# Kernel tuning notes

Measured on AMD Instinct MI355X. Metric: run time of the kernel, lower is better.

Reference implementation:

```python
import jax, jax.numpy as jnp
import numpy as np

HIDDEN = 4096
NUM_EXPERTS = 64
TOP_K = 2


def setup_inputs() -> dict:
    key = jax.random.key(0)
    k1, k2, k3 = jax.random.split(key, 3)
    hidden_states = jax.random.normal(k1, (4, 4096, HIDDEN), dtype=jnp.float32)
    # nn.Linear(hidden_size, num_experts): weight [num_experts, hidden], bias [num_experts]
    bound = 1.0 / np.sqrt(HIDDEN)
    gate_w = jax.random.uniform(k2, (NUM_EXPERTS, HIDDEN), dtype=jnp.float32, minval=-bound, maxval=bound)
    gate_b = jax.random.uniform(k3, (NUM_EXPERTS,), dtype=jnp.float32, minval=-bound, maxval=bound)
    return {"hidden_states": hidden_states, "gate_w": gate_w, "gate_b": gate_b}


def reference(hidden_states, gate_w, gate_b):
    b, s, h = hidden_states.shape
    x = hidden_states.reshape(-1, h)                      # [N, H], N = b*s
    router_logits = jnp.einsum('nh,eh->ne', x, gate_w) + gate_b  # [N, E]
    top_logits, selected_experts = jax.lax.top_k(router_logits, TOP_K)  # [N, K]
    routing_weights = jax.nn.softmax(top_logits, axis=-1)  # [N, K]
    aux_loss = jnp.float32(0.0)
    return routing_weights, selected_experts, router_logits, aux_loss
```

## Files before the change

kernel.cpp:

```cpp
#include <hip/hip_runtime.h>
#include <math.h>
#include <stdint.h>

#define HIDDEN 4096
#define NEXP   64
#define TOKS   64
#define KBLK   2048
#define KCH    64
#define NCHK   (KBLK / KCH)
#define X_FL   (TOKS * KCH)
#define PAR_FL (X_FL + 2 * 2048)

typedef __bf16 bf16x8 __attribute__((ext_vector_type(8)));
typedef float  f32x4  __attribute__((ext_vector_type(4)));

union BfU { uint4 u; bf16x8 b; };

static __device__ __forceinline__ void cvt_hilo(const float* x8, bf16x8& hi, bf16x8& lo) {
#pragma unroll
    for (int j = 0; j < 8; ++j) {
        const float x = x8[j];
        const __bf16 h = (__bf16)x;
        const float  r = x - (float)h;
        hi[j] = h;
        lo[j] = (__bf16)r;
    }
}

__device__ __forceinline__ void gload_lds16(const void* g, void* l) {
    __builtin_amdgcn_global_load_lds(
        (const __attribute__((address_space(1))) void*)g,
        (__attribute__((address_space(3))) void*)l, 16, 0, 0);
}

__global__ __launch_bounds__(512) void wconv_kernel(
    const float* __restrict__ W, ushort* __restrict__ wsHi, ushort* __restrict__ wsLo)
{
    const int gid = blockIdx.x * blockDim.x + threadIdx.x;
    const int S = gid >> 8;
    const int e = (gid >> 6) & 3;
    const int l = gid & 63;
    const int row = 16 * e + (l & 15);
    const int k0  = 32 * S + 8 * (l >> 4);
    const float* src = W + (size_t)row * HIDDEN + k0;
    float x8[8];
    *(float4*)&x8[0] = *(const float4*)src;
    *(float4*)&x8[4] = *(const float4*)(src + 4);
    BfU hi, lo;
    cvt_hilo(x8, hi.b, lo.b);
    const size_t o = ((size_t)(S * 4 + e) * 64 + l) * 8;
    *(uint4*)(wsHi + o) = hi.u;
    *(uint4*)(wsLo + o) = lo.u;
}

__global__ __launch_bounds__(512, 2) void gemm_half_kernel(
    const float* __restrict__ X,
    const ushort* __restrict__ wsHi, const ushort* __restrict__ wsLo,
    float* __restrict__ outLog, float* __restrict__ wsP, int nTok)
{
    __shared__ float smem[2 * PAR_FL];

    const int tid = threadIdx.x;
    const int wv  = tid >> 6;
    const int tg  = wv >> 1;
    const int kh  = wv & 1;
    const int l   = tid & 63;
    const int g   = l >> 4;
    const int cr  = l & 15;
    const int bx  = blockIdx.x;
    const int h   = bx & 1;
    const int t0  = (bx >> 1) * TOKS;

    const float* XgS[2];
    int xdst[2];
#pragma unroll
    for (int r = 0; r < 2; ++r) {
        const int q    = 2 * wv + r;
        const int srow = 4 * q + (l >> 4);
        const int sgr  = (l & 8) | ((l & 7) ^ (srow & 7));
        XgS[r]  = X + (size_t)(t0 + srow) * HIDDEN + h * KBLK + sgr * 4;
        xdst[r] = 4 * q * KCH;
    }
    const ushort* BhS = wsHi + (size_t)h * 131072 + (size_t)wv * 512 + (size_t)l * 8;
    const ushort* BlS = wsLo + (size_t)h * 131072 + (size_t)wv * 512 + (size_t)l * 8;
    const int bhdst = X_FL + wv * 256;
    const int bldst = X_FL + 2048 + wv * 256;

    const int m8   = cr & 7;
    const int rowX = (16 * tg + cr) * KCH;
    const int gA0  = (8 * kh + ((2 * g + 0) ^ m8)) << 2;
    const int gA1  = (8 * kh + ((2 * g + 1) ^ m8)) << 2;

    f32x4 acc[4] = {{0.f,0.f,0.f,0.f},{0.f,0.f,0.f,0.f},{0.f,0.f,0.f,0.f},{0.f,0.f,0.f,0.f}};

#pragma unroll
    for (int r = 0; r < 2; ++r) gload_lds16(XgS[r], smem + xdst[r]);
    gload_lds16(BhS, smem + bhdst);
    gload_lds16(BlS, smem + bldst);
#pragma unroll
    for (int r = 0; r < 2; ++r) gload_lds16(XgS[r] + KCH, smem + PAR_FL + xdst[r]);
    gload_lds16(BhS + 4096, smem + PAR_FL + bhdst);
    gload_lds16(BlS + 4096, smem + PAR_FL + bldst);

#pragma unroll 1
    for (int c = 0; c < NCHK; ++c) {
        if (c + 1 < NCHK) asm volatile("s_waitcnt vmcnt(4)" ::: "memory");
        else              asm volatile("s_waitcnt vmcnt(0)" ::: "memory");
        __builtin_amdgcn_s_barrier();
        const int p = c & 1;
        {
            const float*  xb = smem + p * PAR_FL;
            const ushort* bh = (const ushort*)(xb + X_FL) + (4 * kh) * 512 + l * 8;
            const ushort* bl = bh + 4096;
            float x8[8];
            *(float4*)&x8[0] = *(const float4*)(xb + rowX + gA0);
            *(float4*)&x8[4] = *(const float4*)(xb + rowX + gA1);
            bf16x8 xh, xo; cvt_hilo(x8, xh, xo);
#pragma unroll
            for (int e = 0; e < 4; ++e) {
                BfU ph, pl;
                ph.u = *(const uint4*)(bh + e * 512);
                pl.u = *(const uint4*)(bl + e * 512);
                acc[e] = __builtin_amdgcn_mfma_f32_16x16x32_bf16(xh, ph.b, acc[e], 0, 0, 0);
                acc[e] = __builtin_amdgcn_mfma_f32_16x16x32_bf16(xo, ph.b, acc[e], 0, 0, 0);
                acc[e] = __builtin_amdgcn_mfma_f32_16x16x32_bf16(xh, pl.b, acc[e], 0, 0, 0);
            }
        }
        __builtin_amdgcn_s_barrier();
        if (c + 2 < NCHK) {
            float* pb = smem + p * PAR_FL;
            const int ko = (c + 2) * KCH;
            const size_t bo = (size_t)(c + 2) * 4096;
#pragma unroll
            for (int r = 0; r < 2; ++r) gload_lds16(XgS[r] + ko, pb + xdst[r]);
            gload_lds16(BhS + bo, pb + bhdst);
            gload_lds16(BlS + bo, pb + bldst);
        }
    }

    __syncthreads();

    float (*tiles)[64][68] = (float (*)[64][68])smem;
#pragma unroll
    for (int e = 0; e < 4; ++e)
#pragma unroll
        for (int i = 0; i < 4; ++i)
            tiles[kh][16 * tg + 4 * g + i][16 * e + cr] = acc[e][i];
    __syncthreads();

    {
        float* dst = (h ? wsP : outLog) + (size_t)t0 * NEXP;
        const int tok = tid >> 3;
        const int e8  = (tid & 7) * 8;
        float v[8];
#pragma unroll
        for (int j = 0; j < 8; ++j)
            v[j] = tiles[0][tok][e8 + j] + tiles[1][tok][e8 + j];
        float* rowp = dst + (size_t)tok * NEXP + e8;
        *(float4*)rowp       = make_float4(v[0], v[1], v[2], v[3]);
        *(float4*)(rowp + 4) = make_float4(v[4], v[5], v[6], v[7]);
    }
}

__global__ __launch_bounds__(256) void combine_kernel(
    const float* __restrict__ wsP,
    const float* __restrict__ Bv,
    float* __restrict__ out, int nTok)
{
    __shared__ float tt[64 * 65];
    const int tid = threadIdx.x;
    const int t0  = blockIdx.x * TOKS;
    const size_t offSel = (size_t)nTok * 2;
    const size_t offLog = (size_t)nTok * 4;
    float*       L = out + offLog + (size_t)t0 * NEXP;
    const float* P = wsP + (size_t)t0 * NEXP;

#pragma unroll
    for (int r = 0; r < 4; ++r) {
        const int idx = r * 256 + tid;
        const int tok = idx >> 4;
        const int e4  = (idx & 15) * 4;
        const float4 a  = *(const float4*)(L + tok * NEXP + e4);
        const float4 b  = *(const float4*)(P + tok * NEXP + e4);
        const float4 bb = *(const float4*)(Bv + e4);
        const float4 s = make_float4(a.x + b.x + bb.x, a.y + b.y + bb.y,
                                     a.z + b.z + bb.z, a.w + b.w + bb.w);
        *(float4*)(L + tok * NEXP + e4) = s;
        tt[(e4 + 0) * 65 + tok] = s.x;
        tt[(e4 + 1) * 65 + tok] = s.y;
        tt[(e4 + 2) * 65 + tok] = s.z;
        tt[(e4 + 3) * 65 + tok] = s.w;
    }
    __syncthreads();

    if (tid < 64) {
        const int t = tid;
        float m1 = -INFINITY, m2 = -INFINITY;
        int i1 = 0, i2 = 0;
#pragma unroll
        for (int e = 0; e < NEXP; ++e) {
            const float v = tt[e * 65 + t];
            if (v > m1)      { m2 = m1; i2 = i1; m1 = v; i1 = e; }
            else if (v > m2) { m2 = v; i2 = e; }
        }
        const float ex  = expf(m2 - m1);
        const float inv = 1.0f / (1.0f + ex);
        *(float2*)(out + (size_t)(t0 + tid) * 2)          = make_float2(inv, ex * inv);
        *(float2*)(out + offSel + (size_t)(t0 + tid) * 2) = make_float2((float)i1, (float)i2);
    }

    if (blockIdx.x == 0 && tid == 0)
        out[offLog + (size_t)nTok * NEXP] = 0.0f;
}

extern "C" void kernel_launch(void* const* d_in, const int* in_sizes, int n_in,
                              void* d_out, int out_size, void* d_ws, size_t ws_size,
                              hipStream_t stream)
{
    const float* X  = (const float*)d_in[0];
    const float* W  = (const float*)d_in[1];
    const float* Bv = (const float*)d_in[2];
    float* out = (float*)d_out;
    const int nTok  = in_sizes[0] / HIDDEN;
    const int tiles = nTok / TOKS;
    ushort* wsHi = (ushort*)d_ws;
    ushort* wsLo = wsHi + (size_t)NEXP * HIDDEN;
    float*  wsP  = (float*)(wsLo + (size_t)NEXP * HIDDEN);
    float*  outLog = out + (size_t)nTok * 4;

    wconv_kernel<<<256, 128, 0, stream>>>(W, wsHi, wsLo);
    gemm_half_kernel<<<2 * tiles, 512, 0, stream>>>(X, wsHi, wsLo, outLog, wsP, nTok);
    combine_kernel<<<tiles, 256, 0, stream>>>(wsP, Bv, out, nTok);
}
```

Measured before the change: 67.03 us.

## Split K four ways and divide experts across waves in the gating GEMM

The K dimension is now split into four partial blocks instead of two, giving four times the number of token tiles in blocks. Within a block the waves no longer split K between them; each pair of waves splits the 64 experts, which removes the in-block reduction. Chunks shrink to 32 so shared memory fits more blocks per CU (launch bounds now ask for 4). The cost is three partial logit buffers that the combine kernel must read and sum, which adds extra global traffic.

```diff
diff --git a/kernel.cpp b/kernel.cpp
--- a/kernel.cpp
+++ b/kernel.cpp
@@ -5,11 +5,12 @@
 #define HIDDEN 4096
 #define NEXP   64
 #define TOKS   64
-#define KBLK   2048
-#define KCH    64
+#define NSPLIT 4
+#define KBLK   (HIDDEN / NSPLIT)
+#define KCH    32
 #define NCHK   (KBLK / KCH)
 #define X_FL   (TOKS * KCH)
-#define PAR_FL (X_FL + 2 * 2048)
+#define PAR_FL (X_FL + 2 * 1024)
 
 typedef __bf16 bf16x8 __attribute__((ext_vector_type(8)));
 typedef float  f32x4  __attribute__((ext_vector_type(4)));
@@ -33,7 +34,7 @@
         (__attribute__((address_space(3))) void*)l, 16, 0, 0);
 }
 
-__global__ __launch_bounds__(512) void wconv_kernel(
+__global__ __launch_bounds__(128) void wconv_kernel(
     const float* __restrict__ W, ushort* __restrict__ wsHi, ushort* __restrict__ wsLo)
 {
     const int gid = blockIdx.x * blockDim.x + threadIdx.x;
@@ -53,7 +54,7 @@
     *(uint4*)(wsLo + o) = lo.u;
 }
 
-__global__ __launch_bounds__(512, 2) void gemm_half_kernel(
+__global__ __launch_bounds__(512, 4) void gemm_q_kernel(
     const float* __restrict__ X,
     const ushort* __restrict__ wsHi, const ushort* __restrict__ wsLo,
     float* __restrict__ outLog, float* __restrict__ wsP, int nTok)
@@ -63,61 +64,51 @@
     const int tid = threadIdx.x;
     const int wv  = tid >> 6;
     const int tg  = wv >> 1;
-    const int kh  = wv & 1;
+    const int eh  = wv & 1;
     const int l   = tid & 63;
     const int g   = l >> 4;
     const int cr  = l & 15;
     const int bx  = blockIdx.x;
-    const int h   = bx & 1;
-    const int t0  = (bx >> 1) * TOKS;
-
-    const float* XgS[2];
-    int xdst[2];
-#pragma unroll
-    for (int r = 0; r < 2; ++r) {
-        const int q    = 2 * wv + r;
-        const int srow = 4 * q + (l >> 4);
-        const int sgr  = (l & 8) | ((l & 7) ^ (srow & 7));
-        XgS[r]  = X + (size_t)(t0 + srow) * HIDDEN + h * KBLK + sgr * 4;
-        xdst[r] = 4 * q * KCH;
-    }
-    const ushort* BhS = wsHi + (size_t)h * 131072 + (size_t)wv * 512 + (size_t)l * 8;
-    const ushort* BlS = wsLo + (size_t)h * 131072 + (size_t)wv * 512 + (size_t)l * 8;
-    const int bhdst = X_FL + wv * 256;
-    const int bldst = X_FL + 2048 + wv * 256;
+    const int h   = bx & 3;
+    const int t0  = (bx >> 2) * TOKS;
+
+    const int srow = 8 * wv + (l >> 3);
+    const int sgr  = (l & 7) ^ (l >> 3);
+    const float* XgS = X + (size_t)(t0 + srow) * HIDDEN + h * KBLK + sgr * 4;
+    const int xdst  = wv * 256;
+
+    const ushort* BS = (wv < 4 ? wsHi : wsLo)
+                     + (size_t)h * 65536 + (size_t)(wv & 3) * 512 + (size_t)l * 8;
+    const int bdst = X_FL + (wv < 4 ? 0 : 1024) + (wv & 3) * 256;
 
     const int m8   = cr & 7;
     const int rowX = (16 * tg + cr) * KCH;
-    const int gA0  = (8 * kh + ((2 * g + 0) ^ m8)) << 2;
-    const int gA1  = (8 * kh + ((2 * g + 1) ^ m8)) << 2;
-
-    f32x4 acc[4] = {{0.f,0.f,0.f,0.f},{0.f,0.f,0.f,0.f},{0.f,0.f,0.f,0.f},{0.f,0.f,0.f,0.f}};
-
-#pragma unroll
-    for (int r = 0; r < 2; ++r) gload_lds16(XgS[r], smem + xdst[r]);
-    gload_lds16(BhS, smem + bhdst);
-    gload_lds16(BlS, smem + bldst);
-#pragma unroll
-    for (int r = 0; r < 2; ++r) gload_lds16(XgS[r] + KCH, smem + PAR_FL + xdst[r]);
-    gload_lds16(BhS + 4096, smem + PAR_FL + bhdst);
-    gload_lds16(BlS + 4096, smem + PAR_FL + bldst);
+    const int gA0  = ((2 * g + 0) ^ m8) << 2;
+    const int gA1  = ((2 * g + 1) ^ m8) << 2;
+
+    f32x4 acc[2] = {{0.f,0.f,0.f,0.f},{0.f,0.f,0.f,0.f}};
+
+    gload_lds16(XgS, smem + xdst);
+    gload_lds16(BS, smem + bdst);
+    gload_lds16(XgS + KCH, smem + PAR_FL + xdst);
+    gload_lds16(BS + 2048, smem + PAR_FL + bdst);
 
 #pragma unroll 1
     for (int c = 0; c < NCHK; ++c) {
-        if (c + 1 < NCHK) asm volatile("s_waitcnt vmcnt(4)" ::: "memory");
+        if (c + 1 < NCHK) asm volatile("s_waitcnt vmcnt(2)" ::: "memory");
         else              asm volatile("s_waitcnt vmcnt(0)" ::: "memory");
         __builtin_amdgcn_s_barrier();
         const int p = c & 1;
         {
             const float*  xb = smem + p * PAR_FL;
-            const ushort* bh = (const ushort*)(xb + X_FL) + (4 * kh) * 512 + l * 8;
-            const ushort* bl = bh + 4096;
+            const ushort* bh = (const ushort*)(xb + X_FL) + (2 * eh) * 512 + l * 8;
+            const ushort* bl = bh + 2048;
             float x8[8];
             *(float4*)&x8[0] = *(const float4*)(xb + rowX + gA0);
             *(float4*)&x8[4] = *(const float4*)(xb + rowX + gA1);
             bf16x8 xh, xo; cvt_hilo(x8, xh, xo);
 #pragma unroll
-            for (int e = 0; e < 4; ++e) {
+            for (int e = 0; e < 2; ++e) {
                 BfU ph, pl;
                 ph.u = *(const uint4*)(bh + e * 512);
                 pl.u = *(const uint4*)(bl + e * 512);
@@ -129,36 +120,30 @@
         __builtin_amdgcn_s_barrier();
         if (c + 2 < NCHK) {
             float* pb = smem + p * PAR_FL;
-            const int ko = (c + 2) * KCH;
-            const size_t bo = (size_t)(c + 2) * 4096;
-#pragma unroll
-            for (int r = 0; r < 2; ++r) gload_lds16(XgS[r] + ko, pb + xdst[r]);
-            gload_lds16(BhS + bo, pb + bhdst);
-            gload_lds16(BlS + bo, pb + bldst);
+            gload_lds16(XgS + (c + 2) * KCH, pb + xdst);
+            gload_lds16(BS + (size_t)(c + 2) * 2048, pb + bdst);
         }
     }
 
     __syncthreads();
 
-    float (*tiles)[64][68] = (float (*)[64][68])smem;
-#pragma unroll
-    for (int e = 0; e < 4; ++e)
+    float (*tiles)[68] = (float (*)[68])smem;
+#pragma unroll
+    for (int e = 0; e < 2; ++e) {
+        const int e2 = 2 * eh + e;
 #pragma unroll
         for (int i = 0; i < 4; ++i)
-            tiles[kh][16 * tg + 4 * g + i][16 * e + cr] = acc[e][i];
+            tiles[16 * tg + 4 * g + i][16 * e2 + cr] = acc[e][i];
+    }
     __syncthreads();
 
     {
-        float* dst = (h ? wsP : outLog) + (size_t)t0 * NEXP;
+        float* dst = (h ? wsP + (size_t)(h - 1) * nTok * NEXP : outLog) + (size_t)t0 * NEXP;
         const int tok = tid >> 3;
         const int e8  = (tid & 7) * 8;
-        float v[8];
-#pragma unroll
-        for (int j = 0; j < 8; ++j)
-            v[j] = tiles[0][tok][e8 + j] + tiles[1][tok][e8 + j];
         float* rowp = dst + (size_t)tok * NEXP + e8;
-        *(float4*)rowp       = make_float4(v[0], v[1], v[2], v[3]);
-        *(float4*)(rowp + 4) = make_float4(v[4], v[5], v[6], v[7]);
+        *(float4*)rowp       = *(const float4*)&tiles[tok][e8];
+        *(float4*)(rowp + 4) = *(const float4*)&tiles[tok][e8 + 4];
     }
 }
 
@@ -172,8 +157,9 @@
     const int t0  = blockIdx.x * TOKS;
     const size_t offSel = (size_t)nTok * 2;
     const size_t offLog = (size_t)nTok * 4;
-    float*       L = out + offLog + (size_t)t0 * NEXP;
-    const float* P = wsP + (size_t)t0 * NEXP;
+    const size_t psz    = (size_t)nTok * NEXP;
+    float*       L  = out + offLog + (size_t)t0 * NEXP;
+    const float* P1 = wsP + (size_t)t0 * NEXP;
 
 #pragma unroll
     for (int r = 0; r < 4; ++r) {
@@ -181,10 +167,14 @@
         const int tok = idx >> 4;
         const int e4  = (idx & 15) * 4;
         const float4 a  = *(const float4*)(L + tok * NEXP + e4);
-        const float4 b  = *(const float4*)(P + tok * NEXP + e4);
+        const float4 b  = *(const float4*)(P1 + tok * NEXP + e4);
+        const float4 c  = *(const float4*)(P1 + psz + tok * NEXP + e4);
+        const float4 d  = *(const float4*)(P1 + 2 * psz + tok * NEXP + e4);
         const float4 bb = *(const float4*)(Bv + e4);
-        const float4 s = make_float4(a.x + b.x + bb.x, a.y + b.y + bb.y,
-                                     a.z + b.z + bb.z, a.w + b.w + bb.w);
+        const float4 s = make_float4(a.x + b.x + c.x + d.x + bb.x,
+                                     a.y + b.y + c.y + d.y + bb.y,
+                                     a.z + b.z + c.z + d.z + bb.z,
+                                     a.w + b.w + c.w + d.w + bb.w);
         *(float4*)(L + tok * NEXP + e4) = s;
         tt[(e4 + 0) * 65 + tok] = s.x;
         tt[(e4 + 1) * 65 + tok] = s.y;
@@ -229,6 +219,6 @@
     float*  outLog = out + (size_t)nTok * 4;
 
     wconv_kernel<<<256, 128, 0, stream>>>(W, wsHi, wsLo);
-    gemm_half_kernel<<<2 * tiles, 512, 0, stream>>>(X, wsHi, wsLo, outLog, wsP, nTok);
+    gemm_q_kernel<<<NSPLIT * tiles, 512, 0, stream>>>(X, wsHi, wsLo, outLog, wsP, nTok);
     combine_kernel<<<tiles, 256, 0, stream>>>(wsP, Bv, out, nTok);
 }
```

After: 70.93 us. 1.06x slower.
